# Performance work log

Hardware: AMD Instinct MI355X
Metric: run time of the kernel (lower is better)

## Reference

```python
import jax, jax.numpy as jnp
import numpy as np

MNIST_IM_SIZE = 784
LATENT = 128
BATCH_SIZE = 8192
ETA = 1.0
GAMMA = 1.0
EPS8 = 1e-8


def setup_inputs() -> dict:
    key = jax.random.key(0)
    ks = jax.random.split(key, 8)
    s = 0.02  # weight init scale
    H = MNIST_IM_SIZE * 4          # 3136
    D2 = MNIST_IM_SIZE // 2        # 392
    return {
        "x": jax.random.uniform(ks[0], (BATCH_SIZE, MNIST_IM_SIZE), jnp.float32),
        "eps": jax.random.normal(ks[1], (BATCH_SIZE, LATENT), jnp.float32),
        "W11": jax.random.normal(ks[2], (MNIST_IM_SIZE, H), jnp.float32) * s,
        "b11": jnp.zeros((H,), jnp.float32),
        "W31": jax.random.normal(ks[3], (H, LATENT), jnp.float32) * s,
        "b31": jnp.zeros((LATENT,), jnp.float32),
        "W32": jax.random.normal(ks[4], (H, LATENT), jnp.float32) * s,
        "b32": jnp.zeros((LATENT,), jnp.float32),
        "W44": jax.random.normal(ks[5], (LATENT, D2), jnp.float32) * s,
        "b44": jnp.zeros((D2,), jnp.float32),
        "W61": jax.random.normal(ks[6], (D2, MNIST_IM_SIZE), jnp.float32) * s,
        "b61": jnp.zeros((MNIST_IM_SIZE,), jnp.float32),
    }


def _clog(t):
    # torch BCELoss clamps log at -100
    return jnp.clip(jnp.log(t), -100.0)


def reference(x, eps, W11, b11, W31, b31, W32, b32, W44, b44, W61, b61):
    b2 = BATCH_SIZE // 2

    def encode(xi):
        enc = jax.nn.relu(xi @ W11 + b11)            # [b2, 4*IM]
        mu = jax.nn.relu(enc @ W31 + b31)            # [b2, LATENT]
        sigma = jax.nn.relu(enc @ W32 + b32)         # [b2, LATENT]
        return mu, sigma

    def decode(z):
        dec = jax.nn.relu(z @ W44 + b44)             # [b2, IM/2]
        dec = jax.nn.relu(dec @ W61 + b61)           # [b2, IM]
        return jax.nn.sigmoid(dec)

    x1, x2 = x[:b2], x[b2:]
    mu1, sig1 = encode(x1)
    mu2, sig2 = encode(x2)
    z1 = eps[:b2] * sig1 + mu1
    z2 = eps[b2:] * sig2 + mu2
    y = jnp.concatenate([decode(z1), decode(z2)], axis=0)  # [B, IM]

    # ---- MAE_loss ----
    sigma1 = sig1 + EPS8
    sigma2 = sig2 + EPS8
    rec_loss = -jnp.sum(x * _clog(y) + (1.0 - x) * _clog(1.0 - y))

    sig_m = (sigma1 + sigma2) * 0.5
    mu_m = (mu1 + mu2) * 0.5
    dkl_pq = 0.5 * jnp.sum(-1.0 - jnp.log(EPS8 + sig_m ** 2) + mu_m ** 2 + sig_m ** 2, axis=1)  # [b2]

    # Covariances are diagonal (as_strided diag copy) -> closed forms:
    # inv_cov = diag(1/sigma); det = prod(sigma); trace(inv_cov2 @ cov1) = sum(sigma1/sigma2)
    det1 = jnp.prod(sigma1, axis=1)                  # [b2]
    det2 = jnp.prod(sigma2, axis=1)                  # [b2]
    trace = jnp.sum(sigma1 / sigma2, axis=1)         # [b2]
    diff = mu2 - mu1
    dquad = jnp.sum(diff * diff / sigma2, axis=1)    # [b2]  (diff^T inv_cov2 diff)
    e = jnp.log(EPS8 + det2 / (det1 + EPS8)) - LATENT  # [b2]

    # torch broadcasting artifact: [b2,1,1]+[b2]+[b2] -> [b2,1,b2] -> resize(b2,b2)
    # => D[i,j] = 0.5*(dquad[i] + trace[j] + e[j])
    D = 0.5 * (dquad[:, None] + trace[None, :] + e[None, :])  # [b2, b2]

    l_diverse = jnp.sum(jnp.log1p(jnp.exp(-D)), axis=1)       # [b2]
    mean_qq = jnp.mean(D, axis=1)                             # [b2]
    # torch (b2,b2) - (b2,) broadcasts mean over the LAST axis (per column)
    l_smooth = jnp.sqrt(jnp.sum((D - mean_qq) ** 2, axis=1) / (LATENT - 1))

    loss = rec_loss + jnp.sum(dkl_pq) + ETA * jnp.sum(l_diverse) + GAMMA * jnp.sum(l_smooth)
    return y, loss
```

## Files before the change

kernel.cpp:

```cpp
#include <hip/hip_runtime.h>
#include <hip/hip_bf16.h>
#include <math.h>

#define BATCH   8192
#define IM      784
#define HDIM    3136
#define LAT     128
#define D2      392
#define B2      4096

#define IM_P    800
#define HDIM_P  3200
#define N2_P    256
#define D2_P    512
#define IM_NP   896
#define KSPLIT  4
#define K2S     (HDIM_P / KSPLIT)
#define REC_BLOCKS ((IM_NP / 128) * (BATCH / 128))

typedef __attribute__((ext_vector_type(8))) short short8;
typedef __attribute__((ext_vector_type(4))) float f32x4;

__device__ __forceinline__ void async_load16(const __hip_bfloat16* g, __hip_bfloat16* l)
{
    __builtin_amdgcn_global_load_lds(
        (const __attribute__((address_space(1))) unsigned int*)g,
        (__attribute__((address_space(3))) unsigned int*)l,
        16, 0, 0);
}

template <int L>
__device__ __forceinline__ void wait_prev(int rem)
{
    if (rem >= 1) asm volatile("s_waitcnt vmcnt(%0)" :: "i"(L) : "memory");
    else          asm volatile("s_waitcnt vmcnt(0)" ::: "memory");
}
#define RAW_BARRIER() asm volatile("s_barrier" ::: "memory")

#define PB_X    3200
#define PB_W11  (PB_X   + 2500)
#define PB_W3   (PB_W11 + 800)
#define PB_W44  (PB_W3  + 64)
#define PB_W61  (PB_W44 + 448)
#define PB_END  (PB_W61 + 13)

__device__ __forceinline__ void transpose_tile(
    const float* __restrict__ in, __hip_bfloat16* __restrict__ out,
    int K, int N, int K_pad, int N_pad, int bx, int by, int tid)
{
    __shared__ float tile[32][33];
    int k0 = bx * 32, n0 = by * 32;
    int tx = tid & 31, ty = tid >> 5;
    #pragma unroll
    for (int j = 0; j < 4; ++j) {
        int k = k0 + ty + j * 8, n = n0 + tx;
        tile[ty + j * 8][tx] = (k < K && n < N) ? in[(size_t)k * N + n] : 0.f;
    }
    __syncthreads();
    #pragma unroll
    for (int j = 0; j < 4; ++j) {
        int n = n0 + ty + j * 8, k = k0 + tx;
        if (n < N_pad && k < K_pad)
            out[(size_t)n * K_pad + k] = __float2bfloat16(tile[tx][ty + j * 8]);
    }
}

__global__ __launch_bounds__(256)
void prep(const float* __restrict__ x,
          const float* __restrict__ W11, const float* __restrict__ W31,
          const float* __restrict__ W32, const float* __restrict__ W44,
          const float* __restrict__ W61,
          const float* __restrict__ b11, const float* __restrict__ b31,
          const float* __restrict__ b32, const float* __restrict__ b44,
          const float* __restrict__ b61,
          __hip_bfloat16* __restrict__ x_bf, __hip_bfloat16* __restrict__ W11T,
          __hip_bfloat16* __restrict__ W3xT, __hip_bfloat16* __restrict__ W44T,
          __hip_bfloat16* __restrict__ W61T,
          float* __restrict__ b11p, float* __restrict__ b3x,
          float* __restrict__ b44p, float* __restrict__ b61p)
{
    const int bid = blockIdx.x, tid = threadIdx.x;
    if (bid < PB_X) {
        int gid = bid * 256 + tid;
        int m = gid / 100, ch = gid % 100;
        short8 v = {};
        if (ch < 98) {
            const float* src = x + (size_t)m * IM + ch * 8;
            float4 f0 = *reinterpret_cast<const float4*>(src);
            float4 f1 = *reinterpret_cast<const float4*>(src + 4);
            float f[8] = {f0.x, f0.y, f0.z, f0.w, f1.x, f1.y, f1.z, f1.w};
            #pragma unroll
            for (int k = 0; k < 8; ++k) {
                __hip_bfloat16 h = __float2bfloat16(f[k]);
                v[k] = *reinterpret_cast<short*>(&h);
            }
        }
        *reinterpret_cast<short8*>(&x_bf[(size_t)m * IM_P + ch * 8]) = v;
    } else if (bid < PB_W11) {
        int r = bid - PB_X;
        transpose_tile(W11, W11T, IM, HDIM, IM_P, HDIM_P, r % 25, r / 25, tid);
    } else if (bid < PB_W3) {
        int r = bid - PB_W11;
        int zz = r / 400; r %= 400;
        transpose_tile(zz ? W32 : W31, W3xT + (size_t)zz * 128 * HDIM_P,
                       HDIM, LAT, HDIM_P, 128, r % 100, r / 100, tid);
    } else if (bid < PB_W44) {
        int r = bid - PB_W3;
        transpose_tile(W44, W44T, LAT, D2, LAT, D2_P, r % 4, r / 4, tid);
    } else if (bid < PB_W61) {
        int r = bid - PB_W44;
        transpose_tile(W61, W61T, D2, IM, D2_P, IM_NP, r % 16, r / 16, tid);
    } else {
        int i = (bid - PB_W61) * 256 + tid;
        if (i < HDIM_P) b11p[i] = (i < HDIM) ? b11[i] : 0.f;
        if (i < LAT) { b3x[i] = b31[i]; b3x[LAT + i] = b32[i]; }
        if (i < D2_P) b44p[i] = (i < D2) ? b44[i] : 0.f;
        if (i < IM_NP) b61p[i] = (i < IM) ? b61[i] : 0.f;
    }
}

template <int BN, typename OutT, bool SIGMOID, bool FUSE_REC>
__global__ __launch_bounds__(256)
void gemm_mfma(const __hip_bfloat16* __restrict__ A, const __hip_bfloat16* __restrict__ BT,
               const float* __restrict__ bias, OutT* __restrict__ C,
               int K_pad, int N_logical, int ldc,
               const float* __restrict__ xin, double* __restrict__ rec_arr)
{
    constexpr int NI = BN / 32;
    constexpr int SL = (BN == 128) ? 4 : 3;
    __shared__ alignas(16) __hip_bfloat16 As[2][128 * 32];
    __shared__ alignas(16) __hip_bfloat16 Bs[2][BN * 32];
    __shared__ float shr[4];

    const int t    = threadIdx.x;
    const int wave = t >> 6;
    const int lane = t & 63;
    const int wr   = wave >> 1;
    const int wc   = wave & 1;

    const int nwg = gridDim.x * gridDim.y;
    const int wg  = blockIdx.y * gridDim.x + blockIdx.x;
    const int swz = (wg & 7) * (nwg >> 3) + (wg >> 3);
    const int m0  = (swz / gridDim.x) * 128;
    const int n0  = (swz % gridDim.x) * BN;

    const int srow = lane & 15;
    const int skc  = lane >> 4;
    const __hip_bfloat16* Ag = A + (size_t)(m0 + wave * 32 + srow) * K_pad + skc * 8;
    const __hip_bfloat16* Bg;
    if constexpr (BN == 128)
        Bg = BT + (size_t)(n0 + wave * 32 + srow) * K_pad + skc * 8;
    else
        Bg = BT + (size_t)(n0 + wave * 16 + srow) * K_pad + skc * 8;

    auto stage = [&](int buf, int kt) {
        async_load16(Ag + kt, &As[buf][(wave * 2 + 0) * 512]);
        async_load16(Ag + (size_t)16 * K_pad + kt, &As[buf][(wave * 2 + 1) * 512]);
        if constexpr (BN == 128) {
            async_load16(Bg + kt, &Bs[buf][(wave * 2 + 0) * 512]);
            async_load16(Bg + (size_t)16 * K_pad + kt, &Bs[buf][(wave * 2 + 1) * 512]);
        } else {
            async_load16(Bg + kt, &Bs[buf][wave * 512]);
        }
    };

    f32x4 acc[4][NI] = {};
    const int nt = K_pad >> 5;

    stage(0, 0);

    for (int tt = 0; tt < nt; ++tt) {
        if (tt + 1 < nt) stage((tt + 1) & 1, (tt + 1) << 5);
        wait_prev<SL>(nt - 1 - tt);
        __builtin_amdgcn_sched_barrier(0);
        RAW_BARRIER();

        const int cur = tt & 1;
        short8 af[4], bfv[NI];
        #pragma unroll
        for (int mi = 0; mi < 4; ++mi)
            af[mi] = *reinterpret_cast<const short8*>(&As[cur][(wr * 4 + mi) * 512 + lane * 8]);
        #pragma unroll
        for (int ni = 0; ni < NI; ++ni)
            bfv[ni] = *reinterpret_cast<const short8*>(&Bs[cur][(wc * NI + ni) * 512 + lane * 8]);

        #pragma unroll
        for (int mi = 0; mi < 4; ++mi)
            #pragma unroll
            for (int ni = 0; ni < NI; ++ni)
                acc[mi][ni] = __builtin_amdgcn_mfma_f32_16x16x32_bf16(
                    af[mi], bfv[ni], acc[mi][ni], 0, 0, 0);

        RAW_BARRIER();
    }

    const int fr   = lane & 15;
    const int row4 = (lane >> 4) * 4;
    float rsum = 0.f;
    #pragma unroll
    for (int ni = 0; ni < NI; ++ni) {
        int gn = n0 + wc * (BN / 2) + ni * 16 + fr;
        if (gn >= N_logical) continue;
        float bv = bias[gn];
        #pragma unroll
        for (int mi = 0; mi < 4; ++mi) {
            #pragma unroll
            for (int r = 0; r < 4; ++r) {
                int gm = m0 + wr * 64 + mi * 16 + row4 + r;
                float o = acc[mi][ni][r] + bv;
                o = fmaxf(o, 0.f);
                if (SIGMOID) o = 1.f / (1.f + expf(-o));
                if constexpr (sizeof(OutT) == 2)
                    C[(size_t)gm * ldc + gn] = __float2bfloat16(o);
                else
                    C[(size_t)gm * ldc + gn] = o;
                if constexpr (FUSE_REC) {
                    float xv = xin[(size_t)gm * ldc + gn];
                    float l1 = fmaxf(__logf(o), -100.f);
                    float l2 = fmaxf(__logf(1.f - o), -100.f);
                    rsum += xv * l1 + (1.f - xv) * l2;
                }
            }
        }
    }
    if constexpr (FUSE_REC) {
        for (int off = 32; off; off >>= 1) rsum += __shfl_down(rsum, off);
        if (lane == 0) shr[wave] = rsum;
        __syncthreads();
        if (t == 0)
            rec_arr[wg] = (double)(-(shr[0] + shr[1] + shr[2] + shr[3]));
    }
}

__global__ __launch_bounds__(256)
void gemm_mfma_splitk(const __hip_bfloat16* __restrict__ A, const __hip_bfloat16* __restrict__ BT,
                      float* __restrict__ partial, int K_pad)
{
    constexpr int BN = 64, NI = 2, SL = 3;
    __shared__ alignas(16) __hip_bfloat16 As[2][128 * 32];
    __shared__ alignas(16) __hip_bfloat16 Bs[2][BN * 32];

    const int t    = threadIdx.x;
    const int wave = t >> 6;
    const int lane = t & 63;
    const int wr   = wave >> 1;
    const int wc   = wave & 1;

    const int nwg = gridDim.x * gridDim.y;
    const int wg  = blockIdx.y * gridDim.x + blockIdx.x;
    const int swz = (wg & 7) * (nwg >> 3) + (wg >> 3);
    const int m0  = (swz / gridDim.x) * 128;
    const int n0  = (swz % gridDim.x) * BN;
    const int koff = blockIdx.z * K2S;

    const int srow = lane & 15;
    const int skc  = lane >> 4;
    const __hip_bfloat16* Ag = A + (size_t)(m0 + wave * 32 + srow) * K_pad + skc * 8 + koff;
    const __hip_bfloat16* Bg = BT + (size_t)(n0 + wave * 16 + srow) * K_pad + skc * 8 + koff;

    auto stage = [&](int buf, int kt) {
        async_load16(Ag + kt, &As[buf][(wave * 2 + 0) * 512]);
        async_load16(Ag + (size_t)16 * K_pad + kt, &As[buf][(wave * 2 + 1) * 512]);
        async_load16(Bg + kt, &Bs[buf][wave * 512]);
    };

    f32x4 acc[4][NI] = {};
    const int nt = K2S >> 5;

    stage(0, 0);

    for (int tt = 0; tt < nt; ++tt) {
        if (tt + 1 < nt) stage((tt + 1) & 1, (tt + 1) << 5);
        wait_prev<SL>(nt - 1 - tt);
        __builtin_amdgcn_sched_barrier(0);
        RAW_BARRIER();

        const int cur = tt & 1;
        short8 af[4], bfv[NI];
        #pragma unroll
        for (int mi = 0; mi < 4; ++mi)
            af[mi] = *reinterpret_cast<const short8*>(&As[cur][(wr * 4 + mi) * 512 + lane * 8]);
        #pragma unroll
        for (int ni = 0; ni < NI; ++ni)
            bfv[ni] = *reinterpret_cast<const short8*>(&Bs[cur][(wc * NI + ni) * 512 + lane * 8]);

        #pragma unroll
        for (int mi = 0; mi < 4; ++mi)
            #pragma unroll
            for (int ni = 0; ni < NI; ++ni)
                acc[mi][ni] = __builtin_amdgcn_mfma_f32_16x16x32_bf16(
                    af[mi], bfv[ni], acc[mi][ni], 0, 0, 0);

        RAW_BARRIER();
    }

    const int fr   = lane & 15;
    const int row4 = (lane >> 4) * 4;
    float* out = partial + (size_t)blockIdx.z * BATCH * 256;
    #pragma unroll
    for (int ni = 0; ni < NI; ++ni) {
        int gn = n0 + wc * 32 + ni * 16 + fr;
        #pragma unroll
        for (int mi = 0; mi < 4; ++mi) {
            #pragma unroll
            for (int r = 0; r < 4; ++r) {
                int gm = m0 + wr * 64 + mi * 16 + row4 + r;
                out[(size_t)gm * 256 + gn] = acc[mi][ni][r];
            }
        }
    }
}

__global__ __launch_bounds__(128)
void reduce_stats(const float* __restrict__ partial, const float* __restrict__ b3x,
                  const float* __restrict__ eps, __hip_bfloat16* __restrict__ z,
                  float* __restrict__ a_out, float* __restrict__ c_out,
                  float* __restrict__ dkl_out)
{
    const int b = blockIdx.x;
    const int j = threadIdx.x;
    const size_t r1 = (size_t)b * 256;
    const size_t r2 = (size_t)(B2 + b) * 256;

    float mu1 = 0.f, sg1 = 0.f, mu2 = 0.f, sg2 = 0.f;
    #pragma unroll
    for (int s = 0; s < KSPLIT; ++s) {
        const float* p = partial + (size_t)s * BATCH * 256;
        mu1 += p[r1 + j];  sg1 += p[r1 + 128 + j];
        mu2 += p[r2 + j];  sg2 += p[r2 + 128 + j];
    }
    const float bm = b3x[j], bs = b3x[128 + j];
    mu1 = fmaxf(mu1 + bm, 0.f); sg1 = fmaxf(sg1 + bs, 0.f);
    mu2 = fmaxf(mu2 + bm, 0.f); sg2 = fmaxf(sg2 + bs, 0.f);
    z[(size_t)b * LAT + j]        = __float2bfloat16(fmaf(eps[(size_t)b * LAT + j], sg1, mu1));
    z[(size_t)(B2 + b) * LAT + j] = __float2bfloat16(fmaf(eps[(size_t)(B2 + b) * LAT + j], sg2, mu2));

    float s1 = sg1 + 1e-8f, s2 = sg2 + 1e-8f;
    float sm = 0.5f * (s1 + s2), mm = 0.5f * (mu1 + mu2);
    float dkl = -1.f - logf(1e-8f + sm * sm) + mm * mm + sm * sm;
    float tr  = s1 / s2;
    float df  = mu2 - mu1;
    float dq  = df * df / s2;
    float p1  = s1, p2 = s2;

    for (int off = 32; off; off >>= 1) {
        dkl += __shfl_down(dkl, off);
        tr  += __shfl_down(tr, off);
        dq  += __shfl_down(dq, off);
        p1  *= __shfl_down(p1, off);
        p2  *= __shfl_down(p2, off);
    }
    __shared__ float sh[5][2];
    const int wid = j >> 6;
    if ((j & 63) == 0) { sh[0][wid] = dkl; sh[1][wid] = tr; sh[2][wid] = dq;
                         sh[3][wid] = p1;  sh[4][wid] = p2; }
    __syncthreads();
    if (j == 0) {
        dkl = sh[0][0] + sh[0][1];
        tr  = sh[1][0] + sh[1][1];
        dq  = sh[2][0] + sh[2][1];
        p1  = sh[3][0] * sh[3][1];
        p2  = sh[4][0] * sh[4][1];
        float e = logf(1e-8f + p2 / (p1 + 1e-8f)) - (float)LAT;
        a_out[b]   = 0.5f * dq;
        c_out[b]   = 0.5f * (tr + e);
        dkl_out[b] = 0.5f * dkl;
    }
}

__global__ __launch_bounds__(1024)
void moments_kernel(const float* __restrict__ a, const float* __restrict__ c,
                    const float* __restrict__ dkl, double* __restrict__ accs)
{
    __shared__ double sh[4][16];
    const int tid = threadIdx.x, wid = tid >> 6, lane = tid & 63;
    double sd = 0.0, p1 = 0.0, p2 = 0.0, q = 0.0;
    #pragma unroll
    for (int k = 0; k < 4; ++k) {
        int i = tid + k * 1024;
        double av = a[i], cv = c[i];
        sd += dkl[i];
        p1 += cv;
        p2 += av;
        double d = cv - av;
        q  += d * d;
    }
    for (int off = 32; off; off >>= 1) {
        sd += __shfl_down(sd, off);
        p1 += __shfl_down(p1, off);
        p2 += __shfl_down(p2, off);
        q  += __shfl_down(q, off);
    }
    if (lane == 0) { sh[0][wid] = sd; sh[1][wid] = p1; sh[2][wid] = p2; sh[3][wid] = q; }
    __syncthreads();
    if (tid == 0) {
        double SD = 0, P1 = 0, P2 = 0, Q = 0;
        for (int w = 0; w < 16; ++w) { SD += sh[0][w]; P1 += sh[1][w]; P2 += sh[2][w]; Q += sh[3][w]; }
        double cbar = P1 / (double)B2;
        accs[1] = SD;
        accs[4] = -P2;
        accs[5] = Q - 2.0 * cbar * (P1 - P2) + (double)B2 * cbar * cbar;
    }
}

__global__ __launch_bounds__(256)
void ldiv_smooth(const float* __restrict__ a, const float* __restrict__ c,
                 const double* __restrict__ accs,
                 float* __restrict__ ld_out, double* __restrict__ sm_out)
{
    __shared__ float cs[B2];
    __shared__ float sh[4];
    int i = blockIdx.x;
    float ai = a[i];
    for (int j = threadIdx.x; j < B2; j += 256) cs[j] = c[j];
    __syncthreads();
    float part = 0.f;
    for (int j = threadIdx.x; j < B2; j += 256) {
        float t = -(ai + cs[j]);
        float r = (t > 0.f) ? (t + log1pf(expf(-t))) : log1pf(expf(t));
        part += r;
    }
    for (int off = 32; off; off >>= 1) part += __shfl_down(part, off);
    int wid = threadIdx.x >> 6;
    if ((threadIdx.x & 63) == 0) sh[wid] = part;
    __syncthreads();
    if (threadIdx.x == 0) {
        ld_out[i] = sh[0] + sh[1] + sh[2] + sh[3];
        double S1 = accs[4], S2 = accs[5];
        double aa = (double)ai;
        double q = ((double)B2 * aa * aa + 2.0 * aa * S1 + S2) / (double)(LAT - 1);
        sm_out[i] = sqrt(fmax(q, 0.0));
    }
}

__global__ __launch_bounds__(1024)
void final_kernel(const double* __restrict__ rec_arr, const float* __restrict__ ld,
                  const double* __restrict__ sm, const double* __restrict__ accs,
                  float* __restrict__ out_loss)
{
    __shared__ double sh[16];
    const int tid = threadIdx.x, wid = tid >> 6, lane = tid & 63;
    double s = 0.0;
    if (tid < REC_BLOCKS) s += rec_arr[tid];
    #pragma unroll
    for (int k = 0; k < 4; ++k) {
        int i = tid + k * 1024;
        s += (double)ld[i] + sm[i];
    }
    for (int off = 32; off; off >>= 1) s += __shfl_down(s, off);
    if (lane == 0) sh[wid] = s;
    __syncthreads();
    if (tid == 0) {
        double tot = accs[1];
        for (int w = 0; w < 16; ++w) tot += sh[w];
        out_loss[0] = (float)tot;
    }
}

extern "C" void kernel_launch(void* const* d_in, const int* in_sizes, int n_in,
                              void* d_out, int out_size, void* d_ws, size_t ws_size,
                              hipStream_t stream)
{
    const float* x   = (const float*)d_in[0];
    const float* eps = (const float*)d_in[1];
    const float* W11 = (const float*)d_in[2];
    const float* b11 = (const float*)d_in[3];
    const float* W31 = (const float*)d_in[4];
    const float* b31 = (const float*)d_in[5];
    const float* W32 = (const float*)d_in[6];
    const float* b32 = (const float*)d_in[7];
    const float* W44 = (const float*)d_in[8];
    const float* b44 = (const float*)d_in[9];
    const float* W61 = (const float*)d_in[10];
    const float* b61 = (const float*)d_in[11];
    float* out = (float*)d_out;

    char* ws = (char*)d_ws;
    size_t off = 0;
    auto alloc = [&](size_t bytes) {
        void* p = ws + off;
        off += (bytes + 255) & ~(size_t)255;
        return p;
    };
    __hip_bfloat16* x_bf    = (__hip_bfloat16*)alloc((size_t)BATCH * IM_P * 2);
    __hip_bfloat16* W11T    = (__hip_bfloat16*)alloc((size_t)HDIM_P * IM_P * 2);
    float*          b11p    = (float*)alloc(HDIM_P * 4);
    __hip_bfloat16* enc     = (__hip_bfloat16*)alloc((size_t)BATCH * HDIM_P * 2);
    __hip_bfloat16* W3xT    = (__hip_bfloat16*)alloc((size_t)N2_P * HDIM_P * 2);
    float*          b3x     = (float*)alloc(N2_P * 4);
    __hip_bfloat16* z_bf    = (__hip_bfloat16*)alloc((size_t)BATCH * LAT * 2);
    __hip_bfloat16* W44T    = (__hip_bfloat16*)alloc((size_t)D2_P * LAT * 2);
    float*          b44p    = (float*)alloc(D2_P * 4);
    __hip_bfloat16* dec     = (__hip_bfloat16*)alloc((size_t)BATCH * D2_P * 2);
    __hip_bfloat16* W61T    = (__hip_bfloat16*)alloc((size_t)IM_NP * D2_P * 2);
    float*          b61p    = (float*)alloc(IM_NP * 4);
    float*          av      = (float*)alloc(B2 * 4);
    float*          cv      = (float*)alloc(B2 * 4);
    float*          dklv    = (float*)alloc(B2 * 4);
    float*          ldv     = (float*)alloc(B2 * 4);
    double*         smv     = (double*)alloc(B2 * 8);
    double*         rec_arr = (double*)alloc(REC_BLOCKS * 8);
    double*         accs    = (double*)alloc(8 * sizeof(double));
    float*          partial = (float*)alloc((size_t)KSPLIT * BATCH * N2_P * 4);

    hipMemsetAsync(accs, 0, 8 * sizeof(double), stream);

    prep<<<PB_END, 256, 0, stream>>>(x, W11, W31, W32, W44, W61,
                                     b11, b31, b32, b44, b61,
                                     x_bf, W11T, W3xT, W44T, W61T,
                                     b11p, b3x, b44p, b61p);

    gemm_mfma<128, __hip_bfloat16, false, false>
        <<<dim3(HDIM_P / 128, BATCH / 128), 256, 0, stream>>>(
        x_bf, W11T, b11p, enc, IM_P, HDIM_P, HDIM_P, nullptr, nullptr);
    gemm_mfma_splitk<<<dim3(N2_P / 64, BATCH / 128, KSPLIT), 256, 0, stream>>>(
        enc, W3xT, partial, HDIM_P);
    reduce_stats<<<B2, 128, 0, stream>>>(partial, b3x, eps, z_bf, av, cv, dklv);
    moments_kernel<<<1, 1024, 0, stream>>>(av, cv, dklv, accs);
    gemm_mfma<128, __hip_bfloat16, false, false>
        <<<dim3(D2_P / 128, BATCH / 128), 256, 0, stream>>>(
        z_bf, W44T, b44p, dec, LAT, D2_P, D2_P, nullptr, nullptr);
    gemm_mfma<128, float, true, true>
        <<<dim3(IM_NP / 128, BATCH / 128), 256, 0, stream>>>(
        dec, W61T, b61p, out, D2_P, IM, IM, x, rec_arr);
    ldiv_smooth<<<B2, 256, 0, stream>>>(av, cv, accs, ldv, smv);
    final_kernel<<<1, 1024, 0, stream>>>(rec_arr, ldv, smv, accs, out + (size_t)BATCH * IM);
}
```

Baseline: 333.2 us.

## Triple-buffer GEMM LDS pipeline and streamline softplus reduction kernel

```diff
diff --git a/kernel.cpp b/kernel.cpp
--- a/kernel.cpp
+++ b/kernel.cpp
@@ -30,10 +30,11 @@
 }
 
 template <int L>
-__device__ __forceinline__ void wait_prev(int rem)
-{
-    if (rem >= 1) asm volatile("s_waitcnt vmcnt(%0)" :: "i"(L) : "memory");
-    else          asm volatile("s_waitcnt vmcnt(0)" ::: "memory");
+__device__ __forceinline__ void wait_tiles2(int rem)
+{
+    if (rem >= 2)      asm volatile("s_waitcnt vmcnt(%0)" :: "i"(2 * L) : "memory");
+    else if (rem == 1) asm volatile("s_waitcnt vmcnt(%0)" :: "i"(L) : "memory");
+    else               asm volatile("s_waitcnt vmcnt(0)" ::: "memory");
 }
 #define RAW_BARRIER() asm volatile("s_barrier" ::: "memory")
 
@@ -128,8 +129,8 @@
 {
     constexpr int NI = BN / 32;
     constexpr int SL = (BN == 128) ? 4 : 3;
-    __shared__ alignas(16) __hip_bfloat16 As[2][128 * 32];
-    __shared__ alignas(16) __hip_bfloat16 Bs[2][BN * 32];
+    __shared__ alignas(16) __hip_bfloat16 As[3][128 * 32];
+    __shared__ alignas(16) __hip_bfloat16 Bs[3][BN * 32];
     __shared__ float shr[4];
 
     const int t    = threadIdx.x;
@@ -168,14 +169,16 @@
     const int nt = K_pad >> 5;
 
     stage(0, 0);
-
+    if (nt > 1) stage(1, 32);
+
+    int cur = 0;
     for (int tt = 0; tt < nt; ++tt) {
-        if (tt + 1 < nt) stage((tt + 1) & 1, (tt + 1) << 5);
-        wait_prev<SL>(nt - 1 - tt);
+        int stg = cur + 2; if (stg >= 3) stg -= 3;
+        if (tt + 2 < nt) stage(stg, (tt + 2) << 5);
+        wait_tiles2<SL>(nt - 1 - tt);
         __builtin_amdgcn_sched_barrier(0);
         RAW_BARRIER();
 
-        const int cur = tt & 1;
         short8 af[4], bfv[NI];
         #pragma unroll
         for (int mi = 0; mi < 4; ++mi)
@@ -192,6 +195,7 @@
                     af[mi], bfv[ni], acc[mi][ni], 0, 0, 0);
 
         RAW_BARRIER();
+        cur = (cur + 1 == 3) ? 0 : cur + 1;
     }
 
     const int fr   = lane & 15;
@@ -237,8 +241,8 @@
                       float* __restrict__ partial, int K_pad)
 {
     constexpr int BN = 64, NI = 2, SL = 3;
-    __shared__ alignas(16) __hip_bfloat16 As[2][128 * 32];
-    __shared__ alignas(16) __hip_bfloat16 Bs[2][BN * 32];
+    __shared__ alignas(16) __hip_bfloat16 As[3][128 * 32];
+    __shared__ alignas(16) __hip_bfloat16 Bs[3][BN * 32];
 
     const int t    = threadIdx.x;
     const int wave = t >> 6;
@@ -268,14 +272,16 @@
     const int nt = K2S >> 5;
 
     stage(0, 0);
-
+    stage(1, 32);
+
+    int cur = 0;
     for (int tt = 0; tt < nt; ++tt) {
-        if (tt + 1 < nt) stage((tt + 1) & 1, (tt + 1) << 5);
-        wait_prev<SL>(nt - 1 - tt);
+        int stg = cur + 2; if (stg >= 3) stg -= 3;
+        if (tt + 2 < nt) stage(stg, (tt + 2) << 5);
+        wait_tiles2<SL>(nt - 1 - tt);
         __builtin_amdgcn_sched_barrier(0);
         RAW_BARRIER();
 
-        const int cur = tt & 1;
         short8 af[4], bfv[NI];
         #pragma unroll
         for (int mi = 0; mi < 4; ++mi)
@@ -292,6 +298,7 @@
                     af[mi], bfv[ni], acc[mi][ni], 0, 0, 0);
 
         RAW_BARRIER();
+        cur = (cur + 1 == 3) ? 0 : cur + 1;
     }
 
     const int fr   = lane & 15;
@@ -408,17 +415,20 @@
                  const double* __restrict__ accs,
                  float* __restrict__ ld_out, double* __restrict__ sm_out)
 {
-    __shared__ float cs[B2];
     __shared__ float sh[4];
     int i = blockIdx.x;
     float ai = a[i];
-    for (int j = threadIdx.x; j < B2; j += 256) cs[j] = c[j];
-    __syncthreads();
     float part = 0.f;
-    for (int j = threadIdx.x; j < B2; j += 256) {
-        float t = -(ai + cs[j]);
-        float r = (t > 0.f) ? (t + log1pf(expf(-t))) : log1pf(expf(t));
-        part += r;
+    const float4* c4 = reinterpret_cast<const float4*>(c);
+    for (int j4 = threadIdx.x; j4 < B2 / 4; j4 += 256) {
+        float4 cc = c4[j4];
+        float cv[4] = {cc.x, cc.y, cc.z, cc.w};
+        #pragma unroll
+        for (int u = 0; u < 4; ++u) {
+            float tv = -(ai + cv[u]);
+            float r = (tv > 0.f) ? (tv + log1pf(__expf(-tv))) : log1pf(__expf(tv));
+            part += r;
+        }
     }
     for (int off = 32; off; off >>= 1) part += __shfl_down(part, off);
     int wid = threadIdx.x >> 6;
```

Result: no change. 336.5 us (+1.0%).
